# Kernel tuning notes

Measured on AMD Instinct MI355X. Metric: run time of the kernel, lower is better.

Reference implementation:

```python
import jax, jax.numpy as jnp
import numpy as np

N = 400000
C_IN = 64
C_OUT = 64
K = 27  # 3x3x3 kernel offsets
EPS = 1e-4


def _subm_conv(feat, nbr_t, W):
    # feat: [N, Cin], nbr_t: [K, N] int32, W: [K, Cin, Cout]
    # rulebook-style gather-GEMM-scatter: accumulate over kernel offsets
    def body(acc, kw):
        Wk, idxk = kw
        return acc + feat[idxk] @ Wk, None
    init = jnp.zeros((feat.shape[0], W.shape[-1]), feat.dtype)
    out, _ = jax.lax.scan(body, init, (W, nbr_t))
    return out


def _bn(x, g, b):
    # BatchNorm1d with track_running_stats=False: always uses batch stats
    m = x.mean(axis=0)
    v = x.var(axis=0)
    return (x - m) * jax.lax.rsqrt(v + EPS) * g + b


def _lrelu(x, slope):
    return jnp.where(x >= 0, x, slope * x)


def setup_inputs() -> dict:
    key = jax.random.key(0)
    ks = jax.random.split(key, 11)
    features = jax.random.normal(ks[0], (N, C_IN), dtype=jnp.float32)
    neighbor_idx = jax.random.randint(ks[1], (N, K), 0, N, dtype=jnp.int32)
    s = 0.05
    W1 = jax.random.normal(ks[2], (K, C_IN, C_OUT), dtype=jnp.float32) * s
    W2 = jax.random.normal(ks[3], (K, C_OUT, C_OUT), dtype=jnp.float32) * s
    W3 = jax.random.normal(ks[4], (K, C_OUT, C_OUT), dtype=jnp.float32) * s
    g1 = jax.random.normal(ks[5], (C_OUT,), dtype=jnp.float32) * 0.1 + 1.0
    b1 = jax.random.normal(ks[6], (C_OUT,), dtype=jnp.float32) * 0.1
    g2 = jax.random.normal(ks[7], (C_OUT,), dtype=jnp.float32) * 0.1 + 1.0
    b2 = jax.random.normal(ks[8], (C_OUT,), dtype=jnp.float32) * 0.1
    g3 = jax.random.normal(ks[9], (C_OUT,), dtype=jnp.float32) * 0.1 + 1.0
    b3 = jax.random.normal(ks[10], (C_OUT,), dtype=jnp.float32) * 0.1
    return {"features": features, "neighbor_idx": neighbor_idx,
            "W1": W1, "g1": g1, "b1": b1,
            "W2": W2, "g2": g2, "b2": b2,
            "W3": W3, "g3": g3, "b3": b3}


def reference(features, neighbor_idx, W1, g1, b1, W2, g2, b2, W3, g3, b3):
    nbr_t = neighbor_idx.T  # [K, N]
    # conv_block1: subm conv -> BN -> LeakyReLU(0.05)
    x = _lrelu(_bn(_subm_conv(features, nbr_t, W1), g1, b1), 0.05)
    res = x
    # conv_block2
    x = _lrelu(_bn(_subm_conv(x, nbr_t, W2), g2, b2), 0.05)
    # conv_block3 (no activation) + norm
    x = _bn(_subm_conv(x, nbr_t, W3), g3, b3)
    # residual add + scn.LeakyReLU (default leakiness = 1/3)
    return _lrelu(x + res, 0.333)
```

## Files before the change

### kernel.cpp

```cpp
#include <hip/hip_runtime.h>
#include <hip/hip_bf16.h>

#define N_PTS 400000
#define KOFF 27
#define AP 72

typedef __attribute__((ext_vector_type(8))) short short8;
typedef __attribute__((ext_vector_type(4))) float float4v;

__device__ __forceinline__ unsigned short f2bf(float f) {
    union { float f; unsigned int u; } a; a.f = f;
    unsigned int u = a.u;
    unsigned int r = (u + 0x7FFFu + ((u >> 16) & 1u)) >> 16;
    return (unsigned short)r;
}

__device__ __forceinline__ float bf2f(unsigned short u) {
    union { unsigned int u; float f; } a; a.u = ((unsigned int)u) << 16;
    return a.f;
}

__global__ void cast_feat_kernel(const float* __restrict__ src,
                                 unsigned short* __restrict__ dst, int n4) {
    int i = blockIdx.x * blockDim.x + threadIdx.x;
    if (i >= n4) return;
    const float4* s4 = (const float4*)src;
    float4 v = s4[i];
    ushort4 o;
    o.x = f2bf(v.x); o.y = f2bf(v.y); o.z = f2bf(v.z); o.w = f2bf(v.w);
    ((ushort4*)dst)[i] = o;
}

__global__ void prep_w_all_kernel(const float* __restrict__ W1,
                                  const float* __restrict__ W2,
                                  const float* __restrict__ W3,
                                  unsigned short* __restrict__ Wt,
                                  float* __restrict__ stats) {
    int i = blockIdx.x * blockDim.x + threadIdx.x;
    if (i < 384) stats[i] = 0.0f;
    if (i >= KOFF * 64 * 64) return;
    int k = i >> 12;
    int co = (i >> 6) & 63;
    int ci = i & 63;
    int src = (k << 12) + (ci << 6) + co;
    const int WS = KOFF * 4096;
    Wt[i] = f2bf(W1[src]);
    Wt[i + WS] = f2bf(W2[src]);
    Wt[i + 2 * WS] = f2bf(W3[src]);
}

__global__ __launch_bounds__(512, 6)
void conv_kernel(const unsigned short* __restrict__ X,
                 const int* __restrict__ nbr,
                 const unsigned short* __restrict__ Wt,
                 float* __restrict__ Y,
                 float* __restrict__ stats) {
    __shared__ unsigned short lds_a[128 * AP];
    __shared__ unsigned short lds_w[64 * AP];
    const int tid = threadIdx.x;
    const int wave = tid >> 6;
    const int lane = tid & 63;
    const int quad = lane >> 4;
    const int l16 = lane & 15;
    const int p0 = blockIdx.x * 128;

    const int sr = tid >> 2;
    const int sq = tid & 3;
    const int wr = tid >> 3;
    const int wc = (tid & 7) << 3;

    float4v acc[4];
    #pragma unroll
    for (int t = 0; t < 4; ++t) acc[t] = (float4v){0.f, 0.f, 0.f, 0.f};

    const long nb = (long)(p0 + sr) * KOFF;
    int gi = nbr[nb];
    int gin = nbr[nb + 1];
    uint4 a0, a1, w0;
    {
        const uint4* srcA = (const uint4*)(X + ((size_t)gi << 6)) + sq * 2;
        a0 = srcA[0];
        a1 = srcA[1];
        w0 = ((const uint4*)Wt)[tid];
    }

    for (int k = 0; k < KOFF; ++k) {
        __syncthreads();
        *(uint4*)(lds_a + sr * AP + sq * 16) = a0;
        *(uint4*)(lds_a + sr * AP + sq * 16 + 8) = a1;
        *(uint4*)(lds_w + wr * AP + wc) = w0;
        if (k < KOFF - 1) {
            const uint4* srcA = (const uint4*)(X + ((size_t)gin << 6)) + sq * 2;
            a0 = srcA[0];
            a1 = srcA[1];
            w0 = ((const uint4*)(Wt + (((size_t)(k + 1)) << 12)))[tid];
            gin = (k < KOFF - 2) ? nbr[nb + k + 2] : 0;
        }
        __syncthreads();
        const int abase = (wave * 16 + l16) * AP + quad * 8;
        #pragma unroll
        for (int ks = 0; ks < 2; ++ks) {
            short8 af = *(const short8*)(lds_a + abase + ks * 32);
            #pragma unroll
            for (int t = 0; t < 4; ++t) {
                short8 bf = *(const short8*)(lds_w + (t * 16 + l16) * AP + ks * 32 + quad * 8);
                acc[t] = __builtin_amdgcn_mfma_f32_16x16x32_bf16(af, bf, acc[t], 0, 0, 0);
            }
        }
    }

    const int row_base = p0 + wave * 16 + quad * 4;
    #pragma unroll
    for (int t = 0; t < 4; ++t) {
        #pragma unroll
        for (int r = 0; r < 4; ++r) {
            Y[(size_t)(row_base + r) * 64 + t * 16 + l16] = acc[t][r];
        }
    }

    __syncthreads();
    float* red = (float*)lds_w;
    if (tid < 128) red[tid] = 0.0f;
    __syncthreads();
    #pragma unroll
    for (int t = 0; t < 4; ++t) {
        float s = acc[t][0] + acc[t][1] + acc[t][2] + acc[t][3];
        float ss = acc[t][0] * acc[t][0] + acc[t][1] * acc[t][1] +
                   acc[t][2] * acc[t][2] + acc[t][3] * acc[t][3];
        s += __shfl_down(s, 32);
        s += __shfl_down(s, 16);
        ss += __shfl_down(ss, 32);
        ss += __shfl_down(ss, 16);
        if (lane < 16) {
            atomicAdd(&red[t * 16 + l16], s);
            atomicAdd(&red[64 + t * 16 + l16], ss);
        }
    }
    __syncthreads();
    if (tid < 128) atomicAdd(&stats[tid], red[tid]);
}

__global__ void bnact_kernel(const float* __restrict__ Y, const float* __restrict__ stats,
                             const float* __restrict__ g, const float* __restrict__ b,
                             unsigned short* __restrict__ Xb, float slope) {
    __shared__ float scale[64], shift[64];
    int tid = threadIdx.x;
    if (tid < 64) {
        float m = stats[tid] * (1.0f / N_PTS);
        float v = stats[64 + tid] * (1.0f / N_PTS) - m * m;
        float rs = rsqrtf(v + 1e-4f);
        float sc = rs * g[tid];
        scale[tid] = sc;
        shift[tid] = b[tid] - m * sc;
    }
    __syncthreads();
    int i = blockIdx.x * blockDim.x + tid;
    const int total = N_PTS * 16;
    if (i >= total) return;
    int cb = (i & 15) << 2;
    float4 y = ((const float4*)Y)[i];
    float o0 = y.x * scale[cb] + shift[cb];
    float o1 = y.y * scale[cb + 1] + shift[cb + 1];
    float o2 = y.z * scale[cb + 2] + shift[cb + 2];
    float o3 = y.w * scale[cb + 3] + shift[cb + 3];
    o0 = o0 >= 0.f ? o0 : slope * o0;
    o1 = o1 >= 0.f ? o1 : slope * o1;
    o2 = o2 >= 0.f ? o2 : slope * o2;
    o3 = o3 >= 0.f ? o3 : slope * o3;
    ushort4 o;
    o.x = f2bf(o0); o.y = f2bf(o1); o.z = f2bf(o2); o.w = f2bf(o3);
    ((ushort4*)Xb)[i] = o;
}

__global__ void bnact_final_kernel(float* __restrict__ Y, const float* __restrict__ stats,
                                   const float* __restrict__ g, const float* __restrict__ b,
                                   const unsigned short* __restrict__ res) {
    __shared__ float scale[64], shift[64];
    int tid = threadIdx.x;
    if (tid < 64) {
        float m = stats[tid] * (1.0f / N_PTS);
        float v = stats[64 + tid] * (1.0f / N_PTS) - m * m;
        float rs = rsqrtf(v + 1e-4f);
        float sc = rs * g[tid];
        scale[tid] = sc;
        shift[tid] = b[tid] - m * sc;
    }
    __syncthreads();
    int i = blockIdx.x * blockDim.x + tid;
    const int total = N_PTS * 16;
    if (i >= total) return;
    int cb = (i & 15) << 2;
    float4 y = ((const float4*)Y)[i];
    ushort4 r4 = ((const ushort4*)res)[i];
    float o0 = y.x * scale[cb] + shift[cb] + bf2f(r4.x);
    float o1 = y.y * scale[cb + 1] + shift[cb + 1] + bf2f(r4.y);
    float o2 = y.z * scale[cb + 2] + shift[cb + 2] + bf2f(r4.z);
    float o3 = y.w * scale[cb + 3] + shift[cb + 3] + bf2f(r4.w);
    o0 = o0 >= 0.f ? o0 : 0.333f * o0;
    o1 = o1 >= 0.f ? o1 : 0.333f * o1;
    o2 = o2 >= 0.f ? o2 : 0.333f * o2;
    o3 = o3 >= 0.f ? o3 : 0.333f * o3;
    float4 o; o.x = o0; o.y = o1; o.z = o2; o.w = o3;
    ((float4*)Y)[i] = o;
}

extern "C" void kernel_launch(void* const* d_in, const int* in_sizes, int n_in,
                              void* d_out, int out_size, void* d_ws, size_t ws_size,
                              hipStream_t stream) {
    const float* feat = (const float*)d_in[0];
    const int* nbr = (const int*)d_in[1];
    const float* W1 = (const float*)d_in[2];
    const float* g1 = (const float*)d_in[3];
    const float* b1 = (const float*)d_in[4];
    const float* W2 = (const float*)d_in[5];
    const float* g2 = (const float*)d_in[6];
    const float* b2 = (const float*)d_in[7];
    const float* W3 = (const float*)d_in[8];
    const float* g3 = (const float*)d_in[9];
    const float* b3 = (const float*)d_in[10];
    float* Y = (float*)d_out;

    char* ws = (char*)d_ws;
    const size_t BF_BYTES = (size_t)N_PTS * 64 * 2;
    unsigned short* B0 = (unsigned short*)ws;
    unsigned short* B1 = (unsigned short*)(ws + BF_BYTES);
    unsigned short* Wt = (unsigned short*)(ws + 2 * BF_BYTES);
    float* stats = (float*)(ws + 2 * BF_BYTES + (size_t)3 * KOFF * 4096 * 2);

    const int WSTRIDE = KOFF * 4096;

    cast_feat_kernel<<<25000, 256, 0, stream>>>(feat, B0, N_PTS * 16);
    prep_w_all_kernel<<<(KOFF * 4096 + 255) / 256, 256, 0, stream>>>(W1, W2, W3, Wt, stats);

    conv_kernel<<<N_PTS / 128, 512, 0, stream>>>(B0, nbr, Wt, Y, stats);
    bnact_kernel<<<25000, 256, 0, stream>>>(Y, stats, g1, b1, B1, 0.05f);
    conv_kernel<<<N_PTS / 128, 512, 0, stream>>>(B1, nbr, Wt + WSTRIDE, Y, stats + 128);
    bnact_kernel<<<25000, 256, 0, stream>>>(Y, stats + 128, g2, b2, B0, 0.05f);
    conv_kernel<<<N_PTS / 128, 512, 0, stream>>>(B0, nbr, Wt + 2 * WSTRIDE, Y, stats + 256);
    bnact_final_kernel<<<25000, 256, 0, stream>>>(Y, stats + 256, g3, b3, B1);
}
```

Baseline: 998.8 us.

## Gather conv operands directly into MFMA registers, drop LDS staging and barriers

The conv kernel no longer stages gathered feature rows and weights through shared memory. Each lane loads its MFMA A fragments straight from global memory using its own neighbour indices, with two-deep register prefetch, and reads weight fragments directly from global or cache. Blocks shrink to 256 threads, with each wave covering 32 rows across two accumulator sets. This removes two __syncthreads per kernel offset and the LDS round trip, at the cost of narrower per-lane 16-byte gathers, repeated weight reads from L1/L2 by every wave, and more registers per thread.

```diff
diff --git a/kernel.cpp b/kernel.cpp
--- a/kernel.cpp
+++ b/kernel.cpp
@@ -3,7 +3,6 @@
 
 #define N_PTS 400000
 #define KOFF 27
-#define AP 72
 
 typedef __attribute__((ext_vector_type(8))) short short8;
 typedef __attribute__((ext_vector_type(4))) float float4v;
@@ -49,84 +48,105 @@
     Wt[i + 2 * WS] = f2bf(W3[src]);
 }
 
-__global__ __launch_bounds__(512, 6)
+__global__ __launch_bounds__(256, 4)
 void conv_kernel(const unsigned short* __restrict__ X,
                  const int* __restrict__ nbr,
                  const unsigned short* __restrict__ Wt,
                  float* __restrict__ Y,
                  float* __restrict__ stats) {
-    __shared__ unsigned short lds_a[128 * AP];
-    __shared__ unsigned short lds_w[64 * AP];
+    __shared__ float red[128];
     const int tid = threadIdx.x;
     const int wave = tid >> 6;
     const int lane = tid & 63;
     const int quad = lane >> 4;
     const int l16 = lane & 15;
     const int p0 = blockIdx.x * 128;
-
-    const int sr = tid >> 2;
-    const int sq = tid & 3;
-    const int wr = tid >> 3;
-    const int wc = (tid & 7) << 3;
-
-    float4v acc[4];
+    const int r0 = p0 + wave * 32 + l16;
+    const int r1 = r0 + 16;
+
+    const int* nb0 = nbr + (size_t)r0 * KOFF;
+    const int* nb1 = nbr + (size_t)r1 * KOFF;
+    const unsigned short* Xq = X + quad * 8;
+
+    float4v acc[2][4];
     #pragma unroll
-    for (int t = 0; t < 4; ++t) acc[t] = (float4v){0.f, 0.f, 0.f, 0.f};
-
-    const long nb = (long)(p0 + sr) * KOFF;
-    int gi = nbr[nb];
-    int gin = nbr[nb + 1];
-    uint4 a0, a1, w0;
+    for (int h = 0; h < 2; ++h)
+        #pragma unroll
+        for (int t = 0; t < 4; ++t) acc[h][t] = (float4v){0.f, 0.f, 0.f, 0.f};
+
+    short8 a00, a01, a10, a11;
+    short8 b00, b01, b10, b11;
     {
-        const uint4* srcA = (const uint4*)(X + ((size_t)gi << 6)) + sq * 2;
-        a0 = srcA[0];
-        a1 = srcA[1];
-        w0 = ((const uint4*)Wt)[tid];
-    }
+        const unsigned short* s0 = Xq + ((size_t)nb0[0] << 6);
+        const unsigned short* s1 = Xq + ((size_t)nb1[0] << 6);
+        a00 = *(const short8*)s0; a01 = *(const short8*)(s0 + 32);
+        a10 = *(const short8*)s1; a11 = *(const short8*)(s1 + 32);
+    }
+    {
+        const unsigned short* s0 = Xq + ((size_t)nb0[1] << 6);
+        const unsigned short* s1 = Xq + ((size_t)nb1[1] << 6);
+        b00 = *(const short8*)s0; b01 = *(const short8*)(s0 + 32);
+        b10 = *(const short8*)s1; b11 = *(const short8*)(s1 + 32);
+    }
+    int ic0 = nb0[2], ic1 = nb1[2];
 
     for (int k = 0; k < KOFF; ++k) {
-        __syncthreads();
-        *(uint4*)(lds_a + sr * AP + sq * 16) = a0;
-        *(uint4*)(lds_a + sr * AP + sq * 16 + 8) = a1;
-        *(uint4*)(lds_w + wr * AP + wc) = w0;
-        if (k < KOFF - 1) {
-            const uint4* srcA = (const uint4*)(X + ((size_t)gin << 6)) + sq * 2;
-            a0 = srcA[0];
-            a1 = srcA[1];
-            w0 = ((const uint4*)(Wt + (((size_t)(k + 1)) << 12)))[tid];
-            gin = (k < KOFF - 2) ? nbr[nb + k + 2] : 0;
-        }
-        __syncthreads();
-        const int abase = (wave * 16 + l16) * AP + quad * 8;
+        int jn0 = 0, jn1 = 0;
+        if (k + 3 < KOFF) { jn0 = nb0[k + 3]; jn1 = nb1[k + 3]; }
+
+        const unsigned short* wk = Wt + ((size_t)k << 12) + l16 * 64 + quad * 8;
         #pragma unroll
         for (int ks = 0; ks < 2; ++ks) {
-            short8 af = *(const short8*)(lds_a + abase + ks * 32);
             #pragma unroll
             for (int t = 0; t < 4; ++t) {
-                short8 bf = *(const short8*)(lds_w + (t * 16 + l16) * AP + ks * 32 + quad * 8);
-                acc[t] = __builtin_amdgcn_mfma_f32_16x16x32_bf16(af, bf, acc[t], 0, 0, 0);
+                short8 bf = *(const short8*)(wk + t * 1024 + ks * 32);
+                acc[0][t] = __builtin_amdgcn_mfma_f32_16x16x32_bf16(
+                    ks ? a01 : a00, bf, acc[0][t], 0, 0, 0);
+                acc[1][t] = __builtin_amdgcn_mfma_f32_16x16x32_bf16(
+                    ks ? a11 : a10, bf, acc[1][t], 0, 0, 0);
             }
         }
-    }
-
-    const int row_base = p0 + wave * 16 + quad * 4;
+
+        if (k + 2 < KOFF) {
+            const unsigned short* s0 = Xq + ((size_t)ic0 << 6);
+            const unsigned short* s1 = Xq + ((size_t)ic1 << 6);
+            a00 = *(const short8*)s0; a01 = *(const short8*)(s0 + 32);
+            a10 = *(const short8*)s1; a11 = *(const short8*)(s1 + 32);
+        }
+        short8 t0;
+        t0 = a00; a00 = b00; b00 = t0;
+        t0 = a01; a01 = b01; b01 = t0;
+        t0 = a10; a10 = b10; b10 = t0;
+        t0 = a11; a11 = b11; b11 = t0;
+        ic0 = jn0; ic1 = jn1;
+    }
+
+    #pragma unroll
+    for (int h = 0; h < 2; ++h) {
+        const int row_base = p0 + wave * 32 + h * 16 + quad * 4;
+        #pragma unroll
+        for (int t = 0; t < 4; ++t) {
+            #pragma unroll
+            for (int r = 0; r < 4; ++r) {
+                Y[(size_t)(row_base + r) * 64 + t * 16 + l16] = acc[h][t][r];
+            }
+        }
+    }
+
+    if (tid < 128) red[tid] = 0.0f;
+    __syncthreads();
     #pragma unroll
     for (int t = 0; t < 4; ++t) {
-        #pragma unroll
-        for (int r = 0; r < 4; ++r) {
-            Y[(size_t)(row_base + r) * 64 + t * 16 + l16] = acc[t][r];
-        }
-    }
-
-    __syncthreads();
-    float* red = (float*)lds_w;
-    if (tid < 128) red[tid] = 0.0f;
-    __syncthreads();
-    #pragma unroll
-    for (int t = 0; t < 4; ++t) {
-        float s = acc[t][0] + acc[t][1] + acc[t][2] + acc[t][3];
-        float ss = acc[t][0] * acc[t][0] + acc[t][1] * acc[t][1] +
-                   acc[t][2] * acc[t][2] + acc[t][3] * acc[t][3];
+        float s = 0.f, ss = 0.f;
+        #pragma unroll
+        for (int h = 0; h < 2; ++h) {
+            #pragma unroll
+            for (int r = 0; r < 4; ++r) {
+                float v = acc[h][t][r];
+                s += v;
+                ss += v * v;
+            }
+        }
         s += __shfl_down(s, 32);
         s += __shfl_down(s, 16);
         ss += __shfl_down(ss, 32);
@@ -232,10 +252,10 @@
     cast_feat_kernel<<<25000, 256, 0, stream>>>(feat, B0, N_PTS * 16);
     prep_w_all_kernel<<<(KOFF * 4096 + 255) / 256, 256, 0, stream>>>(W1, W2, W3, Wt, stats);
 
-    conv_kernel<<<N_PTS / 128, 512, 0, stream>>>(B0, nbr, Wt, Y, stats);
+    conv_kernel<<<N_PTS / 128, 256, 0, stream>>>(B0, nbr, Wt, Y, stats);
     bnact_kernel<<<25000, 256, 0, stream>>>(Y, stats, g1, b1, B1, 0.05f);
-    conv_kernel<<<N_PTS / 128, 512, 0, stream>>>(B1, nbr, Wt + WSTRIDE, Y, stats + 128);
+    conv_kernel<<<N_PTS / 128, 256, 0, stream>>>(B1, nbr, Wt + WSTRIDE, Y, stats + 128);
     bnact_kernel<<<25000, 256, 0, stream>>>(Y, stats + 128, g2, b2, B0, 0.05f);
-    conv_kernel<<<N_PTS / 128, 512, 0, stream>>>(B0, nbr, Wt + 2 * WSTRIDE, Y, stats + 256);
+    conv_kernel<<<N_PTS / 128, 256, 0, stream>>>(B0, nbr, Wt + 2 * WSTRIDE, Y, stats + 256);
     bnact_final_kernel<<<25000, 256, 0, stream>>>(Y, stats + 256, g3, b3, B1);
 }
```

New measurement: 1.954 ms. 1.96x slower.
